# Kernel optimization log

Hardware: AMD Instinct MI355X
Metric: run time of the kernel (lower is better)

The kernel has to match this reference:

```python
import jax, jax.numpy as jnp
import numpy as np

HEADS = 24
HEAD_DIM = 128
COND = 1024      # (512//8)*(512//8)*16//64
TXTLEN = 128
EPS = 1e-6


def setup_inputs() -> dict:
    key = jax.random.key(0)
    ks = jax.random.split(key, 16)
    S, D, R = 2176, 3072, 16
    f = lambda k, shp, s=1.0: jax.random.normal(k, shp, dtype=jnp.float32) * s
    return {
        "hidden_states": f(ks[0], (1, S, D)),
        "Wq": f(ks[1], (D, D), 0.02), "bq": f(ks[2], (D,), 0.02),
        "Wk": f(ks[3], (D, D), 0.02), "bk": f(ks[4], (D,), 0.02),
        "Wv": f(ks[5], (D, D), 0.02), "bv": f(ks[6], (D,), 0.02),
        "q_down": f(ks[7], (R, D), 1.0 / R), "q_up": f(ks[8], (D, R), 0.02),
        "k_down": f(ks[9], (R, D), 1.0 / R), "k_up": f(ks[10], (D, R), 0.02),
        "v_down": f(ks[11], (R, D), 1.0 / R), "v_up": f(ks[12], (D, R), 0.02),
        "norm_q_w": jnp.ones((HEAD_DIM,), jnp.float32),
        "norm_k_w": jnp.ones((HEAD_DIM,), jnp.float32),
        "rope_cos": f(ks[13], (S, HEAD_DIM)),
        "rope_sin": f(ks[14], (S, HEAD_DIM)),
    }


def _rms_norm(x, w):
    # per-head RMSNorm over head_dim
    var = jnp.mean(x * x, axis=-1, keepdims=True)
    return x * jax.lax.rsqrt(var + EPS) * w


def _apply_rope(x, cos, sin):
    # diffusers apply_rotary_emb, use_real=True, unbind_dim=-1 (interleaved pairs)
    xr = x.reshape(*x.shape[:-1], HEAD_DIM // 2, 2)
    x_rot = jnp.stack([-xr[..., 1], xr[..., 0]], axis=-1).reshape(x.shape)
    return x * cos[None, None] + x_rot * sin[None, None]


def _forward(hidden_states, Wq, bq, Wk, bk, Wv, bv,
             q_down, q_up, k_down, k_up, v_down, v_up,
             norm_q_w, norm_k_w, rope_cos, rope_sin):
    B, S, D = hidden_states.shape
    block = S - COND  # scaled_block_size

    # dense QKV projections
    q = hidden_states @ Wq.T + bq
    k = hidden_states @ Wk.T + bk
    v = hidden_states @ Wv.T + bv

    # LoRA on cond segment only (mask zeros all rows outside [block, block+COND))
    pos = jnp.arange(S)
    seg = ((pos >= block) & (pos < block + COND)).astype(hidden_states.dtype)[None, :, None]
    hm = hidden_states * seg
    # lora_weight=1.0, network_alpha/rank = 16/16 = 1.0
    q = q + (hm @ q_down.T) @ q_up.T
    k = k + (hm @ k_down.T) @ k_up.T
    v = v + (hm @ v_down.T) @ v_up.T

    # [B, H, S, hd]
    to_heads = lambda t: t.reshape(B, S, HEADS, HEAD_DIM).transpose(0, 2, 1, 3)
    q, k, v = to_heads(q), to_heads(k), to_heads(v)

    q = _rms_norm(q, norm_q_w)
    k = _rms_norm(k, norm_k_w)

    q = _apply_rope(q, rope_cos, rope_sin)
    k = _apply_rope(k, rope_cos, rope_sin)

    # additive mask: rows < block attend everything; cond rows (n_loras=1)
    # attend only their own cond block
    row, col = pos[:, None], pos[None, :]
    allowed = (row < block) | ((row >= block) & (col >= block))
    bias = jnp.where(allowed, 0.0, -1e20).astype(q.dtype)

    scale = 1.0 / np.sqrt(HEAD_DIM)
    scores = jnp.einsum("bhqd,bhkd->bhqk", q, k) * scale + bias
    attn = jax.nn.softmax(scores, axis=-1)
    out = jnp.einsum("bhqk,bhkd->bhqd", attn, v)

    out = out.transpose(0, 2, 1, 3).reshape(B, S, HEADS * HEAD_DIM)
    return out[:, :block, :]  # hidden_states (use_cond=False)


def reference(hidden_states, Wq, bq, Wk, bk, Wv, bv,
              q_down, q_up, k_down, k_up, v_down, v_up,
              norm_q_w, norm_k_w, rope_cos, rope_sin):
    return _forward(hidden_states, Wq, bq, Wk, bk, Wv, bv,
                    q_down, q_up, k_down, k_up, v_down, v_up,
                    norm_q_w, norm_k_w, rope_cos, rope_sin)
```

## Files before the change

kernel.cpp:

```cpp
#include <hip/hip_runtime.h>
#include <stdint.h>

#define Sq   2176
#define Dm   3072
#define NDm  9216
#define NH   24
#define HDm  128
#define BLKR 1152
#define KVH  1088
#define NT2  34
#define N8HS 835584
#define N8W  1179648
#define NB_CVT   3264
#define NB_W     13824
#define NB_LORAT 256

typedef __attribute__((ext_vector_type(8))) __bf16 bf16x8;
typedef __attribute__((ext_vector_type(4))) float f32x4;
typedef __attribute__((ext_vector_type(8))) unsigned short ushort8;

#define AS1 __attribute__((address_space(1)))
#define AS3 __attribute__((address_space(3)))

__device__ __forceinline__ unsigned short f2bf(float x) {
  unsigned u = __builtin_bit_cast(unsigned, x);
  u += 0x7FFFu + ((u >> 16) & 1u);
  return (unsigned short)(u >> 16);
}
__device__ __forceinline__ float bf2f(unsigned short x) {
  return __builtin_bit_cast(float, (unsigned)x << 16);
}

__global__ __launch_bounds__(256) void prep_kernel(
    const float* __restrict__ hs,
    const float* __restrict__ w0, const float* __restrict__ w1,
    const float* __restrict__ w2,
    const float* __restrict__ k_down, const float* __restrict__ v_down,
    unsigned short* __restrict__ hsb, unsigned short* __restrict__ wb,
    float* __restrict__ tkW, float* __restrict__ tvW) {
  __shared__ float hsl[4 * Dm];
  __shared__ float tl[4][32];
  int bid = blockIdx.x, t = threadIdx.x;

  if (bid < NB_CVT) {
    int i = bid * 256 + t;
    const float4* s4 = (const float4*)hs + (size_t)i * 2;
    float4 a = s4[0], b = s4[1];
    ushort8 o;
    o[0]=f2bf(a.x); o[1]=f2bf(a.y); o[2]=f2bf(a.z); o[3]=f2bf(a.w);
    o[4]=f2bf(b.x); o[5]=f2bf(b.y); o[6]=f2bf(b.z); o[7]=f2bf(b.w);
    *((ushort8*)hsb + i) = o;
    return;
  }
  if (bid < NB_CVT + NB_W) {
    int idx = (bid - NB_CVT) * 256 + t;
    int mat = idx < N8W ? 0 : (idx < 2 * N8W ? 1 : 2);
    int i = idx - mat * N8W;
    const float* src = mat == 0 ? w0 : (mat == 1 ? w1 : w2);
    const float4* s4 = (const float4*)src + (size_t)i * 2;
    float4 a = s4[0], b = s4[1];
    ushort8 o;
    o[0]=f2bf(a.x); o[1]=f2bf(a.y); o[2]=f2bf(a.z); o[3]=f2bf(a.w);
    o[4]=f2bf(b.x); o[5]=f2bf(b.y); o[6]=f2bf(b.z); o[7]=f2bf(b.w);
    *((ushort8*)wb + (size_t)mat * (Dm * (size_t)Dm / 8) + i) = o;
    return;
  }
  int bid2 = bid - (NB_CVT + NB_W);
  int r0 = bid2 * 4;
  for (int e = t; e < 4 * Dm; e += 256)
    hsl[e] = hs[((size_t)BLKR + r0) * Dm + e];
  __syncthreads();
  int dot = t >> 3, part = t & 7;
  int mat = dot >> 4, j = dot & 15;
  const float* down = mat ? v_down : k_down;
  float p0 = 0.f, p1 = 0.f, p2 = 0.f, p3 = 0.f;
  for (int e = part; e < Dm; e += 8) {
    float dv = down[j * Dm + e];
    p0 = fmaf(hsl[e], dv, p0);
    p1 = fmaf(hsl[Dm + e], dv, p1);
    p2 = fmaf(hsl[2 * Dm + e], dv, p2);
    p3 = fmaf(hsl[3 * Dm + e], dv, p3);
  }
#pragma unroll
  for (int d = 1; d < 8; d <<= 1) {
    p0 += __shfl_xor(p0, d, 64);
    p1 += __shfl_xor(p1, d, 64);
    p2 += __shfl_xor(p2, d, 64);
    p3 += __shfl_xor(p3, d, 64);
  }
  if (part == 0) { tl[0][dot] = p0; tl[1][dot] = p1; tl[2][dot] = p2; tl[3][dot] = p3; }
  __syncthreads();
  if (t < 128) {
    int rr = t >> 5, jj = t & 31;
    float v = tl[rr][jj];
    if (jj < 16) tkW[(size_t)(r0 + rr) * 16 + jj] = v;
    else         tvW[(size_t)(r0 + rr) * 16 + (jj - 16)] = v;
  }
}

__global__ __launch_bounds__(256, 4) void gemm_kernel(
    const unsigned short* __restrict__ A,
    const unsigned short* __restrict__ B,
    const float* __restrict__ bq, const float* __restrict__ bk,
    const float* __restrict__ bv,
    const float* __restrict__ tkW, const float* __restrict__ tvW,
    const float* __restrict__ kup, const float* __restrict__ vup,
    const float* __restrict__ nqw, const float* __restrict__ nkw,
    const float* __restrict__ rc, const float* __restrict__ rs,
    unsigned short* __restrict__ qh, unsigned short* __restrict__ kh,
    unsigned short* __restrict__ vtb) {
  __shared__ __attribute__((aligned(16))) unsigned short sm[17408];
  __shared__ float rsum[2][2][64];
  int t = threadIdx.x;
  int wid = t >> 6, lane = t & 63;
  int lr = lane & 15, lg = lane >> 4;
  int wr = wid >> 1, wc = wid & 1;

  int bid = blockIdx.x;
  int wg = (bid & 7) * 129 + (bid >> 3);
  int mt, nt;
  if (wg < 216) { nt = wg / 9; mt = wg % 9; }
  else { int r2 = wg - 216; nt = 24 + r2 / 17; mt = r2 % 17; }
  int m0 = mt * 128, n0 = nt * 128;

  f32x4 acc[4][4];
#pragma unroll
  for (int m = 0; m < 4; m++)
#pragma unroll
    for (int n = 0; n < 4; n++) acc[m][n] = (f32x4){0.f, 0.f, 0.f, 0.f};

  int tr = t >> 3;
  int uu = (t & 7) ^ (tr & 7);
  const unsigned short* pA = A + (size_t)(m0 + tr) * Dm + uu * 8;
  const unsigned short* pB = B + (size_t)(n0 + tr) * Dm + uu * 8;

  int lr7 = lr & 7;
  int baseA = (wr * 64 + lr) * 64;
  int baseB = (wc * 64 + lr) * 64;
  int d0 = (lg ^ lr7) * 8;
  int d1 = ((4 + lg) ^ lr7) * 8;

  for (int kt = 0; kt < Dm / 64; kt++) {
    const int ko = kt * 64;
#pragma unroll
    for (int c = 0; c < 4; c++) {
      __builtin_amdgcn_global_load_lds(
          (const AS1 void*)(pA + (size_t)c * 32 * Dm + ko),
          (AS3 void*)(&sm[c * 2048 + wid * 512]), 16, 0, 0);
      __builtin_amdgcn_global_load_lds(
          (const AS1 void*)(pB + (size_t)c * 32 * Dm + ko),
          (AS3 void*)(&sm[8192 + c * 2048 + wid * 512]), 16, 0, 0);
    }
    __syncthreads();

    bf16x8 a0[4], b0[4];
#pragma unroll
    for (int m = 0; m < 4; m++) a0[m] = *(const bf16x8*)&sm[baseA + m * 1024 + d0];
#pragma unroll
    for (int n = 0; n < 4; n++) b0[n] = *(const bf16x8*)&sm[8192 + baseB + n * 1024 + d0];
#pragma unroll
    for (int m = 0; m < 4; m++)
#pragma unroll
      for (int n = 0; n < 4; n++)
        acc[m][n] = __builtin_amdgcn_mfma_f32_16x16x32_bf16(a0[m], b0[n], acc[m][n], 0, 0, 0);

    bf16x8 a1[4], b1[4];
#pragma unroll
    for (int m = 0; m < 4; m++) a1[m] = *(const bf16x8*)&sm[baseA + m * 1024 + d1];
#pragma unroll
    for (int n = 0; n < 4; n++) b1[n] = *(const bf16x8*)&sm[8192 + baseB + n * 1024 + d1];
#pragma unroll
    for (int m = 0; m < 4; m++)
#pragma unroll
      for (int n = 0; n < 4; n++)
        acc[m][n] = __builtin_amdgcn_mfma_f32_16x16x32_bf16(a1[m], b1[n], acc[m][n], 0, 0, 0);
    __syncthreads();
  }

  int region = nt < 24 ? 0 : (nt < 48 ? 1 : 2);
  int h = region == 0 ? nt : (region == 1 ? nt - 24 : nt - 48);
  int dcol[4];
#pragma unroll
  for (int n = 0; n < 4; n++) dcol[n] = wc * 64 + n * 16 + lr;
  const float* bias = region == 0 ? bq : (region == 1 ? bk : bv);
#pragma unroll
  for (int n = 0; n < 4; n++) {
    float b = bias[h * 128 + dcol[n]];
#pragma unroll
    for (int m = 0; m < 4; m++)
#pragma unroll
      for (int i = 0; i < 4; i++) acc[m][n][i] += b;
  }

  if (region >= 1 && m0 >= BLKR) {
    const float* tW = region == 1 ? tkW : tvW;
    const float* up = region == 1 ? kup : vup;
    int rr = t >> 1, half = t & 1;
    const float* srcT = tW + ((size_t)(m0 - BLKR) + rr) * 16 + half * 8;
    const float* srcU = up + ((size_t)h * 128 + rr) * 16 + half * 8;
    ushort8 vT, vU;
#pragma unroll
    for (int u2 = 0; u2 < 8; u2++) { vT[u2] = f2bf(srcT[u2]); vU[u2] = f2bf(srcU[u2]); }
    ushort8 z = {0, 0, 0, 0, 0, 0, 0, 0};
    *(ushort8*)&sm[(rr * 8 + (half ^ (rr & 7))) * 8] = vT;
    *(ushort8*)&sm[(rr * 8 + ((2 + half) ^ (rr & 7))) * 8] = z;
    *(ushort8*)&sm[8192 + (rr * 8 + (half ^ (rr & 7))) * 8] = vU;
    *(ushort8*)&sm[8192 + (rr * 8 + ((2 + half) ^ (rr & 7))) * 8] = z;
    __syncthreads();
    bf16x8 a0[4], b0[4];
#pragma unroll
    for (int m = 0; m < 4; m++) a0[m] = *(const bf16x8*)&sm[baseA + m * 1024 + d0];
#pragma unroll
    for (int n = 0; n < 4; n++) b0[n] = *(const bf16x8*)&sm[8192 + baseB + n * 1024 + d0];
#pragma unroll
    for (int m = 0; m < 4; m++)
#pragma unroll
      for (int n = 0; n < 4; n++)
        acc[m][n] = __builtin_amdgcn_mfma_f32_16x16x32_bf16(a0[m], b0[n], acc[m][n], 0, 0, 0);
    __syncthreads();
  }

  if (region <= 1) {
    float part[4][4];
#pragma unroll
    for (int m = 0; m < 4; m++)
#pragma unroll
      for (int i = 0; i < 4; i++) {
        float p = acc[m][0][i] * acc[m][0][i] + acc[m][1][i] * acc[m][1][i]
                + acc[m][2][i] * acc[m][2][i] + acc[m][3][i] * acc[m][3][i];
#pragma unroll
        for (int d = 1; d < 16; d <<= 1) p += __shfl_xor(p, d, 64);
        part[m][i] = p;
      }
    if (lr == 0) {
#pragma unroll
      for (int m = 0; m < 4; m++)
#pragma unroll
        for (int i = 0; i < 4; i++) rsum[wr][wc][m * 16 + lg * 4 + i] = part[m][i];
    }
    __syncthreads();
    const float* nw = region == 0 ? nqw : nkw;
    float wv[4];
#pragma unroll
    for (int n = 0; n < 4; n++) wv[n] = nw[dcol[n]];
    unsigned short* dstb = region == 0 ? qh : kh;
    int srows = region == 0 ? BLKR : Sq;
#pragma unroll
    for (int m = 0; m < 4; m++)
#pragma unroll
      for (int i = 0; i < 4; i++) {
        int idx = m * 16 + lg * 4 + i;
        float s2 = rsum[wr][0][idx] + rsum[wr][1][idx];
        float rinv = rsqrtf(s2 * (1.f / 128.f) + 1e-6f);
        int r = m0 + wr * 64 + idx;
#pragma unroll
        for (int n = 0; n < 4; n++) {
          float xn = acc[m][n][i] * rinv * wv[n];
          float xp = __shfl_xor(xn, 1, 64);
          float c = rc[r * 128 + dcol[n]];
          float s = rs[r * 128 + dcol[n]];
          float rot = (dcol[n] & 1) ? xp : -xp;
          dstb[((size_t)h * srows + r) * 128 + dcol[n]] = f2bf(xn * c + rot * s);
        }
      }
  } else {
#pragma unroll
    for (int m = 0; m < 4; m++)
#pragma unroll
      for (int i = 0; i < 4; i++) {
        int rl = wr * 64 + m * 16 + lg * 4 + i;
#pragma unroll
        for (int n = 0; n < 4; n++)
          sm[dcol[n] * 136 + rl] = f2bf(acc[m][n][i]);
      }
    __syncthreads();
    int d = t >> 1, rc0 = (t & 1) * 64;
    unsigned short* dv = vtb + ((size_t)h * 128 + d) * Sq + m0 + rc0;
#pragma unroll
    for (int u = 0; u < 8; u++)
      *(ushort8*)(dv + u * 8) = *(const ushort8*)&sm[d * 136 + rc0 + u * 8];
  }
}

__global__ __launch_bounds__(256) void attn_kernel(
    const unsigned short* __restrict__ qh,
    const unsigned short* __restrict__ kh,
    const unsigned short* __restrict__ vt,
    unsigned short* __restrict__ accW,
    float* __restrict__ lW) {
  int bid = blockIdx.x;
  int wg = (bid & 7) * 108 + (bid >> 3);
  int h = wg / 36, rem = wg % 36;
  int qt = rem >> 1, split = rem & 1;
  int q0 = qt * 64;
  int k0 = split * KVH;

  int t = threadIdx.x;
  int w = t >> 6, lane = t & 63;
  int lr = lane & 15, lg = lane >> 4;

  __shared__ __attribute__((aligned(16))) unsigned short kLds[2][32 * 128];
  __shared__ __attribute__((aligned(16))) unsigned short vLds[2][128 * 32];

  const unsigned short* qb = qh + ((size_t)h * BLKR + q0 + w * 16) * 128;
  bf16x8 aq[4];
#pragma unroll
  for (int m = 0; m < 4; m++)
    aq[m] = *(const bf16x8*)(qb + (size_t)lr * 128 + m * 32 + lg * 8);

  const unsigned short* kh_h = kh + ((size_t)h * Sq + k0) * 128;
  const unsigned short* vt_h = vt + (size_t)h * 128 * Sq + k0;

  const unsigned short* srcK[2];
  const unsigned short* srcV[2];
  int kDst[2], vDst[2];
#pragma unroll
  for (int c = 0; c < 2; c++) {
    int u = c * 256 + t;
    int rK = u >> 4, sK = u & 15;
    srcK[c] = kh_h + (size_t)rK * 128 + ((sK ^ (rK & 7)) * 8);
    kDst[c] = u * 8;
    int rV = u >> 2, sV = u & 3;
    srcV[c] = vt_h + (size_t)rV * Sq + ((sV ^ (rV & 3)) * 8);
    vDst[c] = u * 8;
  }

  auto stage = [&](int kt, int buf) {
#pragma unroll
    for (int c = 0; c < 2; c++)
      __builtin_amdgcn_global_load_lds(
          (const AS1 void*)(srcK[c] + (size_t)kt * 4096),
          (AS3 void*)(&kLds[buf][kDst[c]]), 16, 0, 0);
#pragma unroll
    for (int c = 0; c < 2; c++)
      __builtin_amdgcn_global_load_lds(
          (const AS1 void*)(srcV[c] + (size_t)kt * 32),
          (AS3 void*)(&vLds[buf][vDst[c]]), 16, 0, 0);
  };

  f32x4 acc[8];
#pragma unroll
  for (int o = 0; o < 8; o++) acc[o] = (f32x4){0.f, 0.f, 0.f, 0.f};
  float lsum = 0.f;
  const float sc = 0.08838834764831845f;
  const float L2E = 1.4426950408889634f;
  const float ea = sc * L2E, eb = -10.0f * L2E;

  int lr7 = lr & 7, lr3 = lr & 3;
  int adLo = ((((lg & 1) << 1)) * 16 + lr) * 4;
  int adHi = adLo + 64;
  bool hiKb = (lg & 2) != 0;

  auto compute = [&](int buf) {
    const unsigned short* kbuf = kLds[buf];
    const unsigned short* vbuf = vLds[buf];
    f32x4 s2[2];
    s2[0] = (f32x4){0.f, 0.f, 0.f, 0.f};
    s2[1] = (f32x4){0.f, 0.f, 0.f, 0.f};
    __builtin_amdgcn_s_setprio(1);
#pragma unroll
    for (int kb = 0; kb < 2; kb++)
#pragma unroll
      for (int m = 0; m < 4; m++) {
        bf16x8 kf = *(const bf16x8*)&kbuf[(kb * 16 + lr) * 128 + ((m * 4 + lg) ^ lr7) * 8];
        s2[kb] = __builtin_amdgcn_mfma_f32_16x16x32_bf16(kf, aq[m], s2[kb], 0, 0, 0);
      }
    __builtin_amdgcn_s_setprio(0);
    unsigned pk0[2], pk1[2];
#pragma unroll
    for (int kb = 0; kb < 2; kb++) {
      float p0 = exp2f(fmaf(s2[kb][0], ea, eb));
      float p1 = exp2f(fmaf(s2[kb][1], ea, eb));
      float p2 = exp2f(fmaf(s2[kb][2], ea, eb));
      float p3 = exp2f(fmaf(s2[kb][3], ea, eb));
      lsum += (p0 + p1) + (p2 + p3);
      unsigned r0, r1;
      asm("v_cvt_pk_bf16_f32 %0, %1, %2" : "=v"(r0) : "v"(p0), "v"(p1));
      asm("v_cvt_pk_bf16_f32 %0, %1, %2" : "=v"(r1) : "v"(p2), "v"(p3));
      if (kb == 0) { pk0[0] = r0; pk0[1] = r1; }
      else         { pk1[0] = r0; pk1[1] = r1; }
    }
    int a00 = __builtin_amdgcn_ds_bpermute(adLo, (int)pk0[0]);
    int a01 = __builtin_amdgcn_ds_bpermute(adLo, (int)pk0[1]);
    int a10 = __builtin_amdgcn_ds_bpermute(adLo, (int)pk1[0]);
    int a11 = __builtin_amdgcn_ds_bpermute(adLo, (int)pk1[1]);
    int b00 = __builtin_amdgcn_ds_bpermute(adHi, (int)pk0[0]);
    int b01 = __builtin_amdgcn_ds_bpermute(adHi, (int)pk0[1]);
    int b10 = __builtin_amdgcn_ds_bpermute(adHi, (int)pk1[0]);
    int b11 = __builtin_amdgcn_ds_bpermute(adHi, (int)pk1[1]);
    int4 pw;
    pw.x = hiKb ? a10 : a00;
    pw.y = hiKb ? a11 : a01;
    pw.z = hiKb ? b10 : b00;
    pw.w = hiKb ? b11 : b01;
    bf16x8 pfrag = __builtin_bit_cast(bf16x8, pw);
    __builtin_amdgcn_s_setprio(1);
#pragma unroll
    for (int o = 0; o < 8; o++) {
      bf16x8 vf = *(const bf16x8*)&vbuf[(o * 16 + lr) * 32 + (lg ^ lr3) * 8];
      acc[o] = __builtin_amdgcn_mfma_f32_16x16x32_bf16(vf, pfrag, acc[o], 0, 0, 0);
    }
    __builtin_amdgcn_s_setprio(0);
  };

  stage(0, 0);
  __syncthreads();
  for (int kt = 0; kt < NT2; kt += 2) {
    stage(kt + 1, 1);
    compute(0);
    __syncthreads();
    if (kt + 2 < NT2) stage(kt + 2, 0);
    compute(1);
    __syncthreads();
  }

  lsum += __shfl_xor(lsum, 16, 64);
  lsum += __shfl_xor(lsum, 32, 64);

  unsigned short* accP = accW + (size_t)split * BLKR * 3072;
  size_t rowOff = (size_t)(q0 + w * 16 + lr) * 3072 + h * 128;
#pragma unroll
  for (int o = 0; o < 8; o++) {
    ushort4 o4 = make_ushort4(f2bf(acc[o][0]), f2bf(acc[o][1]),
                              f2bf(acc[o][2]), f2bf(acc[o][3]));
    *(ushort4*)&accP[rowOff + o * 16 + lg * 4] = o4;
  }
  if (lg == 0) {
    float* lP = lW + (size_t)split * NH * BLKR + (size_t)h * BLKR;
    lP[q0 + w * 16 + lr] = lsum;
  }
}

__global__ __launch_bounds__(256) void normalize_kernel(
    const unsigned short* __restrict__ accW, const float* __restrict__ lW,
    float* __restrict__ out) {
  int idx = blockIdx.x * 256 + threadIdx.x;
  int r = idx / 384, rem = idx % 384;
  int c = rem * 8, h = c >> 7;
  ushort8 u0 = *(const ushort8*)(accW + (size_t)r * 3072 + c);
  ushort8 u1 = *(const ushort8*)(accW + (size_t)BLKR * 3072 + (size_t)r * 3072 + c);
  float l = lW[(size_t)h * BLKR + r] + lW[(size_t)NH * BLKR + (size_t)h * BLKR + r];
  float inv = 1.0f / l;
  float4 o0, o1;
  o0.x = (bf2f(u0[0]) + bf2f(u1[0])) * inv;
  o0.y = (bf2f(u0[1]) + bf2f(u1[1])) * inv;
  o0.z = (bf2f(u0[2]) + bf2f(u1[2])) * inv;
  o0.w = (bf2f(u0[3]) + bf2f(u1[3])) * inv;
  o1.x = (bf2f(u0[4]) + bf2f(u1[4])) * inv;
  o1.y = (bf2f(u0[5]) + bf2f(u1[5])) * inv;
  o1.z = (bf2f(u0[6]) + bf2f(u1[6])) * inv;
  o1.w = (bf2f(u0[7]) + bf2f(u1[7])) * inv;
  float4* op = (float4*)(out + (size_t)r * 3072 + c);
  op[0] = o0; op[1] = o1;
}

extern "C" void kernel_launch(void* const* d_in, const int* in_sizes, int n_in,
                              void* d_out, int out_size, void* d_ws, size_t ws_size,
                              hipStream_t stream) {
  const float* hs  = (const float*)d_in[0];
  const float* Wq  = (const float*)d_in[1];
  const float* bq  = (const float*)d_in[2];
  const float* Wk  = (const float*)d_in[3];
  const float* bk  = (const float*)d_in[4];
  const float* Wv  = (const float*)d_in[5];
  const float* bv  = (const float*)d_in[6];
  const float* k_down = (const float*)d_in[9];
  const float* k_up   = (const float*)d_in[10];
  const float* v_down = (const float*)d_in[11];
  const float* v_up   = (const float*)d_in[12];
  const float* nqw = (const float*)d_in[13];
  const float* nkw = (const float*)d_in[14];
  const float* rc  = (const float*)d_in[15];
  const float* rsn = (const float*)d_in[16];
  float* out = (float*)d_out;

  char* ws = (char*)d_ws;
  unsigned short* hsb = (unsigned short*)(ws + 0);
  unsigned short* wb  = (unsigned short*)(ws + 13369344);
  unsigned short* accW = (unsigned short*)(ws + 69992448);
  float* lW   = (float*)(ws + 98304000);
  float* tkW  = (float*)(ws + 98525184);
  float* tvW  = (float*)(ws + 98590720);
  unsigned short* qh  = (unsigned short*)(ws + 150208512);
  unsigned short* kh  = (unsigned short*)(ws + 157286400);
  unsigned short* vtb = (unsigned short*)(ws + 170655744);

  prep_kernel<<<dim3(NB_CVT + NB_W + NB_LORAT), 256, 0, stream>>>(
      hs, Wq, Wk, Wv, k_down, v_down, hsb, wb, tkW, tvW);

  gemm_kernel<<<dim3(1032), 256, 0, stream>>>(hsb, wb, bq, bk, bv,
                                              tkW, tvW, k_up, v_up,
                                              nqw, nkw, rc, rsn, qh, kh, vtb);
  attn_kernel<<<dim3(2 * 18 * NH), 256, 0, stream>>>(qh, kh, vtb, accW, lW);
  normalize_kernel<<<dim3(BLKR * 3072 / 8 / 256), 256, 0, stream>>>(accW, lW, out);
}
```

Measured before the change: 297.6 us.

## Drop split-KV attention and fuse normalization into attention epilogue

```diff
diff --git a/kernel.cpp b/kernel.cpp
--- a/kernel.cpp
+++ b/kernel.cpp
@@ -7,8 +7,7 @@
 #define NH   24
 #define HDm  128
 #define BLKR 1152
-#define KVH  1088
-#define NT2  34
+#define NTF  68
 #define N8HS 835584
 #define N8W  1179648
 #define NB_CVT   3264
@@ -26,9 +25,6 @@
   unsigned u = __builtin_bit_cast(unsigned, x);
   u += 0x7FFFu + ((u >> 16) & 1u);
   return (unsigned short)(u >> 16);
-}
-__device__ __forceinline__ float bf2f(unsigned short x) {
-  return __builtin_bit_cast(float, (unsigned)x << 16);
 }
 
 __global__ __launch_bounds__(256) void prep_kernel(
@@ -286,14 +282,11 @@
     const unsigned short* __restrict__ qh,
     const unsigned short* __restrict__ kh,
     const unsigned short* __restrict__ vt,
-    unsigned short* __restrict__ accW,
-    float* __restrict__ lW) {
+    float* __restrict__ out) {
   int bid = blockIdx.x;
-  int wg = (bid & 7) * 108 + (bid >> 3);
-  int h = wg / 36, rem = wg % 36;
-  int qt = rem >> 1, split = rem & 1;
+  int wg = (bid & 7) * 54 + (bid >> 3);
+  int h = wg / 18, qt = wg % 18;
   int q0 = qt * 64;
-  int k0 = split * KVH;
 
   int t = threadIdx.x;
   int w = t >> 6, lane = t & 63;
@@ -308,8 +301,8 @@
   for (int m = 0; m < 4; m++)
     aq[m] = *(const bf16x8*)(qb + (size_t)lr * 128 + m * 32 + lg * 8);
 
-  const unsigned short* kh_h = kh + ((size_t)h * Sq + k0) * 128;
-  const unsigned short* vt_h = vt + (size_t)h * 128 * Sq + k0;
+  const unsigned short* kh_h = kh + (size_t)h * Sq * 128;
+  const unsigned short* vt_h = vt + (size_t)h * 128 * Sq;
 
   const unsigned short* srcK[2];
   const unsigned short* srcV[2];
@@ -405,53 +398,26 @@
 
   stage(0, 0);
   __syncthreads();
-  for (int kt = 0; kt < NT2; kt += 2) {
+  for (int kt = 0; kt < NTF; kt += 2) {
     stage(kt + 1, 1);
     compute(0);
     __syncthreads();
-    if (kt + 2 < NT2) stage(kt + 2, 0);
+    if (kt + 2 < NTF) stage(kt + 2, 0);
     compute(1);
     __syncthreads();
   }
 
   lsum += __shfl_xor(lsum, 16, 64);
   lsum += __shfl_xor(lsum, 32, 64);
-
-  unsigned short* accP = accW + (size_t)split * BLKR * 3072;
+  float inv = 1.0f / lsum;
+
   size_t rowOff = (size_t)(q0 + w * 16 + lr) * 3072 + h * 128;
 #pragma unroll
   for (int o = 0; o < 8; o++) {
-    ushort4 o4 = make_ushort4(f2bf(acc[o][0]), f2bf(acc[o][1]),
-                              f2bf(acc[o][2]), f2bf(acc[o][3]));
-    *(ushort4*)&accP[rowOff + o * 16 + lg * 4] = o4;
-  }
-  if (lg == 0) {
-    float* lP = lW + (size_t)split * NH * BLKR + (size_t)h * BLKR;
-    lP[q0 + w * 16 + lr] = lsum;
-  }
-}
-
-__global__ __launch_bounds__(256) void normalize_kernel(
-    const unsigned short* __restrict__ accW, const float* __restrict__ lW,
-    float* __restrict__ out) {
-  int idx = blockIdx.x * 256 + threadIdx.x;
-  int r = idx / 384, rem = idx % 384;
-  int c = rem * 8, h = c >> 7;
-  ushort8 u0 = *(const ushort8*)(accW + (size_t)r * 3072 + c);
-  ushort8 u1 = *(const ushort8*)(accW + (size_t)BLKR * 3072 + (size_t)r * 3072 + c);
-  float l = lW[(size_t)h * BLKR + r] + lW[(size_t)NH * BLKR + (size_t)h * BLKR + r];
-  float inv = 1.0f / l;
-  float4 o0, o1;
-  o0.x = (bf2f(u0[0]) + bf2f(u1[0])) * inv;
-  o0.y = (bf2f(u0[1]) + bf2f(u1[1])) * inv;
-  o0.z = (bf2f(u0[2]) + bf2f(u1[2])) * inv;
-  o0.w = (bf2f(u0[3]) + bf2f(u1[3])) * inv;
-  o1.x = (bf2f(u0[4]) + bf2f(u1[4])) * inv;
-  o1.y = (bf2f(u0[5]) + bf2f(u1[5])) * inv;
-  o1.z = (bf2f(u0[6]) + bf2f(u1[6])) * inv;
-  o1.w = (bf2f(u0[7]) + bf2f(u1[7])) * inv;
-  float4* op = (float4*)(out + (size_t)r * 3072 + c);
-  op[0] = o0; op[1] = o1;
+    f32x4 v = acc[o];
+    v[0] *= inv; v[1] *= inv; v[2] *= inv; v[3] *= inv;
+    *(f32x4*)&out[rowOff + o * 16 + lg * 4] = v;
+  }
 }
 
 extern "C" void kernel_launch(void* const* d_in, const int* in_sizes, int n_in,
@@ -477,8 +443,6 @@
   char* ws = (char*)d_ws;
   unsigned short* hsb = (unsigned short*)(ws + 0);
   unsigned short* wb  = (unsigned short*)(ws + 13369344);
-  unsigned short* accW = (unsigned short*)(ws + 69992448);
-  float* lW   = (float*)(ws + 98304000);
   float* tkW  = (float*)(ws + 98525184);
   float* tvW  = (float*)(ws + 98590720);
   unsigned short* qh  = (unsigned short*)(ws + 150208512);
@@ -491,6 +455,5 @@
   gemm_kernel<<<dim3(1032), 256, 0, stream>>>(hsb, wb, bq, bk, bv,
                                               tkW, tvW, k_up, v_up,
                                               nqw, nkw, rc, rsn, qh, kh, vtb);
-  attn_kernel<<<dim3(2 * 18 * NH), 256, 0, stream>>>(qh, kh, vtb, accW, lW);
-  normalize_kernel<<<dim3(BLKR * 3072 / 8 / 256), 256, 0, stream>>>(accW, lW, out);
+  attn_kernel<<<dim3(18 * NH), 256, 0, stream>>>(qh, kh, vtb, out);
 }
```

Result: no change. 297.1 us (-0.1%).
